# Kernel tuning notes

Hardware: AMD Instinct MI355X
Metric: run time of the kernel (lower is better)

Reference implementation:

```python
import jax, jax.numpy as jnp
import numpy as np


def _ortho_matrix(key, d, m):
    # block-orthogonal random matrix with chi-distributed row-norm rescaling
    n_blocks = m // d + (1 if m % d else 0)
    keys = jax.random.split(key, n_blocks + 1)
    blocks = []
    for i in range(m // d):
        q, _ = jnp.linalg.qr(jax.random.normal(keys[i], (d, d), dtype=jnp.float32))
        blocks.append(q)
    rem = m % d
    if rem > 0:
        q, _ = jnp.linalg.qr(jax.random.normal(keys[m // d], (d, d), dtype=jnp.float32))
        blocks.append(q[:, :rem])
    proj = jnp.concatenate(blocks, axis=1)  # [d, m]
    scales = jnp.linalg.norm(jax.random.normal(keys[-1], (m, d), dtype=jnp.float32), axis=1)
    return proj * scales[None, :]


def _feature_map(x, P, eps=1e-6):
    # FAVOR+ positive softmax feature map: [exp(xP - |x|^2/2), exp(-xP - |x|^2/2)]
    proj = x @ P  # [B,N,m]
    xn = 0.5 * jnp.sum(x * x, axis=-1, keepdims=True)
    pos = proj - xn
    neg = -proj - xn
    mx = jnp.maximum(jnp.max(pos, axis=-1, keepdims=True), jnp.max(neg, axis=-1, keepdims=True))
    feats = jnp.concatenate([jnp.exp(pos - mx), jnp.exp(neg - mx)], axis=-1)
    return feats * (2.0 * P.shape[1]) ** -0.5 + eps  # [B,N,2m]


def setup_inputs() -> dict:
    key = jax.random.key(0)
    ks = jax.random.split(key, 16)
    B, C, N = 4, 256, 8192
    da, nb = C // 4, 64
    d_geo, r_geo = 16, 16
    x = jax.random.normal(ks[0], (B, C, N), dtype=jnp.float32)
    pos = jax.random.uniform(ks[1], (B, N, 3), dtype=jnp.float32)
    Wq = jax.random.normal(ks[2], (da, C), dtype=jnp.float32) * (C ** -0.5)
    Wk = jax.random.normal(ks[3], (da, C), dtype=jnp.float32) * (C ** -0.5)
    Wv = jax.random.normal(ks[4], (C, C), dtype=jnp.float32) * (C ** -0.5)
    proj_sm = _ortho_matrix(ks[5], da, nb)  # [da, nb]
    Wg1 = jax.random.normal(ks[6], (d_geo, 3), dtype=jnp.float32) * (3 ** -0.5)
    bg1 = jnp.zeros((d_geo,), dtype=jnp.float32)
    Wg2 = jax.random.normal(ks[7], (d_geo, d_geo), dtype=jnp.float32) * (d_geo ** -0.5)
    bg2 = jnp.zeros((d_geo,), dtype=jnp.float32)
    log_tau = jnp.zeros((), dtype=jnp.float32)
    omega_geo = _ortho_matrix(ks[8], d_geo, r_geo)  # [d_geo, r_geo]
    Wp = jax.random.normal(ks[9], (C, C), dtype=jnp.float32) * (C ** -0.5)
    bn_gamma = jnp.ones((C,), dtype=jnp.float32)
    bn_beta = jnp.zeros((C,), dtype=jnp.float32)
    return {"x": x, "pos": pos, "Wq": Wq, "Wk": Wk, "Wv": Wv, "proj_sm": proj_sm,
            "Wg1": Wg1, "bg1": bg1, "Wg2": Wg2, "bg2": bg2, "log_tau": log_tau,
            "omega_geo": omega_geo, "Wp": Wp, "bn_gamma": bn_gamma, "bn_beta": bn_beta}


def reference(x, pos, Wq, Wk, Wv, proj_sm, Wg1, bg1, Wg2, bg2, log_tau, omega_geo, Wp, bn_gamma, bn_beta):
    eps = 1e-6
    da = Wq.shape[0]
    scale = da ** -0.25
    # 1x1 convs == channel matmuls; transpose to [B,N,*]
    q = jnp.einsum('bcn,oc->bno', x, Wq) * scale
    k = jnp.einsum('bcn,oc->bno', x, Wk) * scale
    v = jnp.einsum('bcn,oc->bno', x, Wv)
    q_p = _feature_map(q, proj_sm, eps)  # [B,N,r_sm]
    k_p = _feature_map(k, proj_sm, eps)
    # GeoRFF: learnable Gaussian RFF on MLP-transformed coordinates
    g = jax.nn.relu(pos @ Wg1.T + bg1) @ Wg2.T + bg2  # [B,N,d_geo]
    tau = jax.nn.softplus(log_tau) + 1e-6
    z = jnp.sqrt(2.0 * tau) * g
    z_proj = z @ omega_geo  # [B,N,r_geo]
    z_norm = 0.5 * jnp.sum(z * z, axis=-1, keepdims=True)
    phi = jnp.exp(z_proj - z_norm) * (omega_geo.shape[1] ** -0.5)  # [B,N,r_geo]
    # outer-product feature combination
    B, N, r_sm = q_p.shape
    r_geo = phi.shape[-1]
    Phi_q = (q_p[..., :, None] * phi[..., None, :]).reshape(B, N, r_sm * r_geo)
    Phi_k = (k_p[..., :, None] * phi[..., None, :]).reshape(B, N, r_sm * r_geo)
    # O(N) linear-attention chain
    kv = jnp.einsum('bnr,bnc->brc', Phi_k, v)         # [B,r,C]
    k_sum = jnp.sum(Phi_k, axis=1)                     # [B,r]
    denom = jnp.einsum('bnr,br->bn', Phi_q, k_sum)[..., None] + eps
    fsa = jnp.einsum('bnr,brc->bnc', Phi_q, kv) / denom  # [B,N,C]
    # offset attention: proj(x - fsa) + x, proj = Conv1x1 -> BN(train stats) -> ReLU
    y = x - jnp.transpose(fsa, (0, 2, 1))  # [B,C,N]
    h = jnp.einsum('bcn,oc->bon', y, Wp)
    mean = jnp.mean(h, axis=(0, 2), keepdims=True)
    var = jnp.var(h, axis=(0, 2), keepdims=True)
    hn = (h - mean) * jax.lax.rsqrt(var + 1e-5) * bn_gamma[None, :, None] + bn_beta[None, :, None]
    return jax.nn.relu(hn) + x
```

## Files before the change

### kernel.cpp

```cpp
#include <hip/hip_runtime.h>
#include <hip/hip_bf16.h>
#include <math.h>

#define BB 4
#define CC 256
#define NN 8192
#define RSM 128
#define RGEO 16

typedef __attribute__((ext_vector_type(8))) short short8v;
typedef __attribute__((ext_vector_type(4))) float f32x4;
typedef __attribute__((ext_vector_type(4))) unsigned int u32x4;

#define MFMA16 __builtin_amdgcn_mfma_f32_16x16x32_bf16

#define P_QP   0ull
#define P_KPT  8388608ull
#define P_PHIR 16777216ull
#define P_PHIT 17825792ull
#define P_XT   18874368ull
#define P_VT   35651584ull
#define P_YNT  35651584ull
#define P_KVT  56623104ull
#define P_DEN  61865984ull
#define P_WQK  61997056ull
#define P_WV   62062592ull
#define P_WP   62193664ull
#define P_PSMT 62324736ull
#define P_BN   62332928ull
#define P_KVF  62337024ull
#define P_H    0ull

__device__ __forceinline__ unsigned short f2bu(float f){
    __hip_bfloat16 h = __float2bfloat16(f);
    return __builtin_bit_cast(unsigned short, h);
}
__device__ __forceinline__ float bu2f(unsigned short u){
    return __builtin_bit_cast(float, ((unsigned int)u) << 16);
}
__device__ __forceinline__ unsigned int pack2(float a, float b){
    return (unsigned int)f2bu(a) | (((unsigned int)f2bu(b)) << 16);
}
__device__ __forceinline__ int swz128(int row, int cb){ return (row*128 + cb) ^ ((row & 7) << 4); }
__device__ __forceinline__ int swz256(int row, int cb){ return (row*256 + cb) ^ ((row & 7) << 4); }

__device__ __forceinline__ void stage64(const unsigned short* __restrict__ g, size_t stride,
                                        char* lds, int t){
    #pragma unroll
    for (int i = 0; i < 2; ++i){
        int id = t + 256*i; int row = id >> 3, q = id & 7;
        short8v v = *(const short8v*)(g + (size_t)row*stride + q*8);
        *(short8v*)(lds + swz128(row, q*16)) = v;
    }
}
__device__ __forceinline__ short8v fld(const char* lds, int row, int cb){
    return *(const short8v*)(lds + swz128(row, cb));
}
__device__ __forceinline__ void mfma8(const char* As, const char* Bs, f32x4 acc[2][2],
                                      int wm, int wn, int lr, int lq){
    #pragma unroll
    for (int kk = 0; kk < 2; ++kk){
        short8v a0 = fld(As, wm*32 + lr,      kk*64 + lq*16);
        short8v a1 = fld(As, wm*32 + 16 + lr, kk*64 + lq*16);
        short8v b0 = fld(Bs, wn*32 + lr,      kk*64 + lq*16);
        short8v b1 = fld(Bs, wn*32 + 16 + lr, kk*64 + lq*16);
        acc[0][0] = MFMA16(a0, b0, acc[0][0], 0, 0, 0);
        acc[0][1] = MFMA16(a0, b1, acc[0][1], 0, 0, 0);
        acc[1][0] = MFMA16(a1, b0, acc[1][0], 0, 0, 0);
        acc[1][1] = MFMA16(a1, b1, acc[1][1], 0, 0, 0);
    }
}

__global__ __launch_bounds__(256) void k_prep(const float* __restrict__ Wq, const float* __restrict__ Wk,
    const float* __restrict__ Wv, const float* __restrict__ Wp, const float* __restrict__ Psm,
    unsigned short* __restrict__ Wqk_bf, unsigned short* __restrict__ Wv_bf,
    unsigned short* __restrict__ Wp_bf, unsigned short* __restrict__ Psm_t,
    unsigned short* __restrict__ v_t)
{
    const int tid = blockIdx.x*256 + threadIdx.x;
    const int nth = 64*256;
    for (int i = tid; i < 32768; i += nth){
        int o = i >> 8, c = i & 255;
        Wqk_bf[i] = f2bu(o < 64 ? Wq[o*256 + c] : Wk[(o-64)*256 + c]);
    }
    for (int i = tid; i < 65536; i += nth) Wv_bf[i] = f2bu(Wv[i]);
    for (int i = tid; i < 65536; i += nth) Wp_bf[i] = f2bu(Wp[i]);
    for (int i = tid; i < 4096; i += nth){
        int m = i >> 6, o = i & 63;
        Psm_t[i] = f2bu(Psm[o*64 + m] * 0.35355339059327373f);
    }
    for (int i = tid; i < BB*64*NN; i += nth){
        int b = i >> 19, rem = i & 524287;
        int row = rem >> 13, n = rem & 8191;
        v_t[((size_t)(b*320 + 256 + row))*NN + n] = (row == 0) ? (unsigned short)0x3F80 : (unsigned short)0;
    }
}

__global__ __launch_bounds__(256) void k_xt(const float* __restrict__ x, unsigned short* __restrict__ xT)
{
    __shared__ float xs[64][65];
    const int t = threadIdx.x;
    const int b  = blockIdx.x >> 9;
    const int ct = (blockIdx.x >> 7) & 3;
    const int nt = blockIdx.x & 127;
    const int c0 = ct*64, n0 = nt*64;
    #pragma unroll
    for (int i = 0; i < 4; ++i){
        int id = t + 256*i; int row = id >> 4, fq = id & 15;
        f32x4 v = *(const f32x4*)(x + ((size_t)(b*CC + c0 + row))*NN + n0 + fq*4);
        xs[row][fq*4+0] = v[0]; xs[row][fq*4+1] = v[1];
        xs[row][fq*4+2] = v[2]; xs[row][fq*4+3] = v[3];
    }
    __syncthreads();
    #pragma unroll
    for (int i = 0; i < 2; ++i){
        int id = t + 256*i; int n = id >> 3, q = id & 7;
        u32x4 o;
        #pragma unroll
        for (int j2 = 0; j2 < 4; ++j2)
            o[j2] = pack2(xs[q*8 + j2*2][n], xs[q*8 + j2*2+1][n]);
        *(u32x4*)(void*)(xT + ((size_t)(b*NN + n0 + n))*CC + c0 + q*8) = o;
    }
}

__global__ __launch_bounds__(256) void k_wgemm(const unsigned short* __restrict__ A,
    const unsigned short* __restrict__ Bsrc, unsigned short* __restrict__ out, int orows)
{
    __shared__ __align__(16) char As[8192];
    __shared__ __align__(16) char Bs[8192];
    const int t = threadIdx.x;
    const int l = t & 63, w = t >> 6, wm = w >> 1, wn = w & 1, lr = l & 15, lq = l >> 4;
    const int b  = blockIdx.x >> 9;
    const int ct = (blockIdx.x >> 7) & 3;
    const int nt = blockIdx.x & 127;
    const int c0 = ct*64, n0 = nt*64;

    f32x4 acc[2][2] = {};
    for (int ks = 0; ks < 4; ++ks){
        stage64(A + (size_t)c0*256 + ks*64, 256, As, t);
        stage64(Bsrc + ((size_t)(b*NN + n0))*256 + ks*64, 256, Bs, t);
        __syncthreads();
        mfma8(As, Bs, acc, wm, wn, lr, lq);
        __syncthreads();
    }
    #pragma unroll
    for (int mi = 0; mi < 2; ++mi)
        #pragma unroll
        for (int ni = 0; ni < 2; ++ni)
            #pragma unroll
            for (int r = 0; r < 4; ++r){
                int c = c0 + wm*32 + mi*16 + lq*4 + r;
                int n = n0 + wn*32 + ni*16 + lr;
                out[((size_t)(b*orows + c))*NN + n] = f2bu(acc[mi][ni][r]);
            }
}

__global__ __launch_bounds__(256) void k_qk(const unsigned short* __restrict__ Wqk,
    const unsigned short* __restrict__ xT, const unsigned short* __restrict__ Psm_t,
    unsigned short* __restrict__ qp, unsigned short* __restrict__ kp_t)
{
    __shared__ __align__(16) char As[16384];
    __shared__ __align__(16) char Bs[8192];
    __shared__ __align__(16) char Ts[16384];
    __shared__ __align__(16) char Ps[8192];
    const int t = threadIdx.x;
    const int l = t & 63, w = t >> 6, wm = w >> 1, wn = w & 1, lr = l & 15, lq = l >> 4;
    const int b  = blockIdx.x >> 7;
    const int nt = blockIdx.x & 127;
    const int n0 = nt*64;

    stage64(Psm_t, 64, Ps, t);

    f32x4 acc[4][2] = {};
    for (int ks = 0; ks < 4; ++ks){
        #pragma unroll
        for (int i = 0; i < 4; ++i){
            int id = t + 256*i; int row = id >> 3, q = id & 7;
            short8v v = *(const short8v*)(Wqk + (size_t)row*256 + ks*64 + q*8);
            *(short8v*)(As + swz128(row, q*16)) = v;
        }
        stage64(xT + ((size_t)(b*NN + n0))*256 + ks*64, 256, Bs, t);
        __syncthreads();
        #pragma unroll
        for (int kk = 0; kk < 2; ++kk){
            short8v b0 = fld(Bs, wn*32 + lr,      kk*64 + lq*16);
            short8v b1 = fld(Bs, wn*32 + 16 + lr, kk*64 + lq*16);
            #pragma unroll
            for (int mi = 0; mi < 4; ++mi){
                short8v a = fld(As, wm*64 + mi*16 + lr, kk*64 + lq*16);
                acc[mi][0] = MFMA16(a, b0, acc[mi][0], 0, 0, 0);
                acc[mi][1] = MFMA16(a, b1, acc[mi][1], 0, 0, 0);
            }
        }
        __syncthreads();
    }
    #pragma unroll
    for (int mi = 0; mi < 4; ++mi)
        #pragma unroll
        for (int ni = 0; ni < 2; ++ni){
            int op = (wm*64 + mi*16 + lq*4)*2;
            int nrow = wn*32 + ni*16 + lr;
            *(unsigned int*)(Ts + swz256(nrow, op))     = pack2(acc[mi][ni][0], acc[mi][ni][1]);
            *(unsigned int*)(Ts + swz256(nrow, op + 4)) = pack2(acc[mi][ni][2], acc[mi][ni][3]);
        }
    __syncthreads();

    const float inv128 = 0.08838834764831845f;
    for (int p = 0; p < 2; ++p){
        f32x4 ac[4] = {};
        #pragma unroll
        for (int kk = 0; kk < 2; ++kk){
            short8v bf = *(const short8v*)(Ts + swz256(w*16 + lr, p*128 + kk*64 + lq*16));
            #pragma unroll
            for (int mi = 0; mi < 4; ++mi){
                short8v a = *(const short8v*)(Ps + swz128(mi*16 + lr, kk*64 + lq*16));
                ac[mi] = MFMA16(a, bf, ac[mi], 0, 0, 0);
            }
        }
        float mx = 0.f;
        #pragma unroll
        for (int mi = 0; mi < 4; ++mi)
            #pragma unroll
            for (int r = 0; r < 4; ++r) mx = fmaxf(mx, fabsf(ac[mi][r]));
        mx = fmaxf(mx, __shfl_xor(mx, 16));
        mx = fmaxf(mx, __shfl_xor(mx, 32));
        const int n = n0 + w*16 + lr;
        if (p == 0){
            unsigned short* qr = qp + ((size_t)(b*NN + n))*RSM;
            #pragma unroll
            for (int mi = 0; mi < 4; ++mi){
                float e0 = __expf( ac[mi][0]-mx)*inv128 + 1e-6f;
                float e1 = __expf( ac[mi][1]-mx)*inv128 + 1e-6f;
                float e2 = __expf( ac[mi][2]-mx)*inv128 + 1e-6f;
                float e3 = __expf( ac[mi][3]-mx)*inv128 + 1e-6f;
                float g0 = __expf(-ac[mi][0]-mx)*inv128 + 1e-6f;
                float g1 = __expf(-ac[mi][1]-mx)*inv128 + 1e-6f;
                float g2 = __expf(-ac[mi][2]-mx)*inv128 + 1e-6f;
                float g3 = __expf(-ac[mi][3]-mx)*inv128 + 1e-6f;
                int i0 = mi*16 + lq*4;
                uint2 pu; pu.x = pack2(e0, e1); pu.y = pack2(e2, e3);
                uint2 nu; nu.x = pack2(g0, g1); nu.y = pack2(g2, g3);
                *(uint2*)(void*)(qr + i0)      = pu;
                *(uint2*)(void*)(qr + 64 + i0) = nu;
            }
        } else {
            unsigned short* kb = kp_t + (size_t)(b*RSM)*NN + n;
            #pragma unroll
            for (int mi = 0; mi < 4; ++mi){
                int i0 = mi*16 + lq*4;
                #pragma unroll
                for (int r = 0; r < 4; ++r){
                    kb[(size_t)(i0 + r)*NN]      = f2bu(__expf( ac[mi][r]-mx)*inv128 + 1e-6f);
                    kb[(size_t)(i0 + r + 64)*NN] = f2bu(__expf(-ac[mi][r]-mx)*inv128 + 1e-6f);
                }
            }
        }
    }
}

__global__ __launch_bounds__(256) void k_phi(const float* __restrict__ pos,
    const float* __restrict__ Wg1, const float* __restrict__ bg1,
    const float* __restrict__ Wg2, const float* __restrict__ bg2,
    const float* __restrict__ log_tau, const float* __restrict__ omega,
    unsigned short* __restrict__ phi_row, unsigned short* __restrict__ phi_t)
{
    const int t = threadIdx.x;
    const int b = blockIdx.x >> 5;
    const int n = ((blockIdx.x & 31) << 8) + t;
    const float* pp = pos + ((size_t)(b*NN + n))*3;
    const float p0 = pp[0], p1 = pp[1], p2 = pp[2];
    float hb[16];
    #pragma unroll
    for (int i = 0; i < 16; ++i)
        hb[i] = fmaxf(0.f, fmaf(Wg1[i*3+0], p0, fmaf(Wg1[i*3+1], p1, fmaf(Wg1[i*3+2], p2, bg1[i]))));
    const float tau = log1pf(__expf(log_tau[0])) + 1e-6f;
    const float sc  = sqrtf(2.f*tau);
    float z[16]; float zn = 0.f;
    #pragma unroll
    for (int i = 0; i < 16; ++i){
        float g = bg2[i];
        #pragma unroll
        for (int j = 0; j < 16; ++j) g = fmaf(Wg2[i*16+j], hb[j], g);
        z[i] = sc*g; zn = fmaf(z[i], z[i], zn);
    }
    zn *= 0.5f;
    float val[16];
    #pragma unroll
    for (int m = 0; m < 16; ++m){
        float s = 0.f;
        #pragma unroll
        for (int i = 0; i < 16; ++i) s = fmaf(z[i], omega[i*16+m], s);
        val[m] = __expf(s - zn)*0.25f;
    }
    unsigned short* pr = phi_row + ((size_t)(b*NN + n))*16;
    u32x4 o0, o1;
    #pragma unroll
    for (int j2 = 0; j2 < 4; ++j2){
        o0[j2] = pack2(val[j2*2], val[j2*2+1]);
        o1[j2] = pack2(val[8+j2*2], val[8+j2*2+1]);
    }
    *(u32x4*)(void*)pr = o0;
    *(u32x4*)(void*)(pr + 8) = o1;
    #pragma unroll
    for (int m = 0; m < 16; ++m)
        phi_t[((size_t)(b*RGEO + m))*NN + n] = f2bu(val[m]);
}

__global__ __launch_bounds__(256) void k_kv(const unsigned short* __restrict__ kp_t,
    const unsigned short* __restrict__ phi_t, const unsigned short* __restrict__ v_t,
    float* __restrict__ kv_f32)
{
    __shared__ __align__(16) char As[8192];
    __shared__ __align__(16) char Bs[8192];
    const int t = threadIdx.x;
    const int l = t & 63, w = t >> 6, wm = w >> 1, wn = w & 1, lr = l & 15, lq = l >> 4;
    const int bid = blockIdx.x;
    const int b   = bid / 640;
    const int rem = bid % 640;
    const int ksl = rem / 160;
    const int rr  = rem % 160;
    const int ct = rr >> 5, rt = rr & 31;
    const int c0 = ct*64, r0 = rt*64;
    const int rl = t >> 2, u = t & 3;
    const int rg = r0 + rl;
    const unsigned short* kpr = kp_t + ((size_t)(b*RSM  + (rg >> 4)))*NN;
    const unsigned short* phr = phi_t + ((size_t)(b*RGEO + (rg & 15)))*NN;

    f32x4 acc[2][2] = {};
    for (int ks = ksl*32; ks < ksl*32 + 32; ++ks){
        const int nk = ks*64;
        stage64(v_t + ((size_t)(b*320 + c0))*NN + nk, NN, As, t);
        {
            const int nb = nk + u*16;
            short8v k0 = *(const short8v*)(kpr + nb);
            short8v k1 = *(const short8v*)(kpr + nb + 8);
            short8v q0 = *(const short8v*)(phr + nb);
            short8v q1 = *(const short8v*)(phr + nb + 8);
            u32x4 o0, o1;
            #pragma unroll
            for (int j2 = 0; j2 < 4; ++j2){
                o0[j2] = pack2(bu2f((unsigned short)k0[j2*2])  *bu2f((unsigned short)q0[j2*2]),
                               bu2f((unsigned short)k0[j2*2+1])*bu2f((unsigned short)q0[j2*2+1]));
                o1[j2] = pack2(bu2f((unsigned short)k1[j2*2])  *bu2f((unsigned short)q1[j2*2]),
                               bu2f((unsigned short)k1[j2*2+1])*bu2f((unsigned short)q1[j2*2+1]));
            }
            *(u32x4*)(Bs + swz128(rl, u*32))      = o0;
            *(u32x4*)(Bs + swz128(rl, u*32 + 16)) = o1;
        }
        __syncthreads();
        mfma8(As, Bs, acc, wm, wn, lr, lq);
        __syncthreads();
    }
    #pragma unroll
    for (int mi = 0; mi < 2; ++mi)
        #pragma unroll
        for (int ni = 0; ni < 2; ++ni)
            #pragma unroll
            for (int r = 0; r < 4; ++r){
                int c = c0 + wm*32 + mi*16 + lq*4 + r;
                int rg2 = r0 + wn*32 + ni*16 + lr;
                atomicAdd(&kv_f32[((size_t)(b*320 + c))*2048 + rg2], acc[mi][ni][r]);
            }
}

__global__ __launch_bounds__(256) void k_kvred(const float* __restrict__ kv_f32,
    unsigned short* __restrict__ kv_t)
{
    const size_t i = ((size_t)blockIdx.x*256 + threadIdx.x)*4;
    f32x4 v = *(const f32x4*)(kv_f32 + i);
    uint2 o; o.x = pack2(v[0], v[1]); o.y = pack2(v[2], v[3]);
    *(uint2*)(void*)(kv_t + i) = o;
}

__global__ __launch_bounds__(256) void k_denom(const unsigned short* __restrict__ qp,
    const unsigned short* __restrict__ phi_row, const unsigned short* __restrict__ kv_t,
    float* __restrict__ den)
{
    __shared__ float ks[2048];
    const int t = threadIdx.x;
    const int b = blockIdx.x >> 5;
    const int n = ((blockIdx.x & 31) << 8) + t;
    const unsigned short* ksrc = kv_t + ((size_t)(b*320 + 256))*2048;
    #pragma unroll
    for (int i = 0; i < 8; ++i){ int idx = t + 256*i; ks[idx] = bu2f(ksrc[idx]); }
    __syncthreads();
    float phf[16];
    {
        const unsigned short* pr = phi_row + ((size_t)(b*NN + n))*16;
        short8v a = *(const short8v*)pr;
        short8v c = *(const short8v*)(pr + 8);
        #pragma unroll
        for (int j = 0; j < 8; ++j){ phf[j] = bu2f((unsigned short)a[j]); phf[8+j] = bu2f((unsigned short)c[j]); }
    }
    const unsigned short* qr = qp + ((size_t)(b*NN + n))*RSM;
    float acc = 0.f;
    for (int i = 0; i < 128; i += 8){
        short8v qv = *(const short8v*)(qr + i);
        #pragma unroll
        for (int ii = 0; ii < 8; ++ii){
            const float* kk = &ks[(i + ii)*16];
            float s = 0.f;
            #pragma unroll
            for (int j = 0; j < 16; ++j) s = fmaf(phf[j], kk[j], s);
            acc = fmaf(bu2f((unsigned short)qv[ii]), s, acc);
        }
    }
    den[b*NN + n] = acc + 1e-6f;
}

__global__ __launch_bounds__(256) void k_fsa(const unsigned short* __restrict__ kv_t,
    const unsigned short* __restrict__ qp, const unsigned short* __restrict__ phi_row,
    const float* __restrict__ den, const unsigned short* __restrict__ xT,
    unsigned short* __restrict__ y_nt)
{
    __shared__ __align__(16) char As[8192];
    __shared__ __align__(16) char Bs[8192];
    __shared__ __align__(16) char Ys[8192];
    const int t = threadIdx.x;
    const int l = t & 63, w = t >> 6, wm = w >> 1, wn = w & 1, lr = l & 15, lq = l >> 4;
    const int b  = blockIdx.x >> 9;
    const int ct = (blockIdx.x >> 7) & 3;
    const int nt = blockIdx.x & 127;
    const int c0 = ct*64, n0 = nt*64;
    const int nl = t >> 2, u = t & 3;

    float phf[16];
    {
        const unsigned short* pr = phi_row + ((size_t)(b*NN + n0 + nl))*16;
        short8v a = *(const short8v*)pr;
        short8v c = *(const short8v*)(pr + 8);
        #pragma unroll
        for (int j = 0; j < 8; ++j){ phf[j] = bu2f((unsigned short)a[j]); phf[8+j] = bu2f((unsigned short)c[j]); }
    }
    const unsigned short* qprow = qp + ((size_t)(b*NN + n0 + nl))*RSM;

    f32x4 acc[2][2] = {};
    for (int ks = 0; ks < 32; ++ks){
        stage64(kv_t + ((size_t)(b*320 + c0))*2048 + ks*64, 2048, As, t);
        {
            float qv = bu2f(qprow[ks*4 + u]);
            u32x4 o0, o1;
            #pragma unroll
            for (int j2 = 0; j2 < 4; ++j2){
                o0[j2] = pack2(qv*phf[j2*2],     qv*phf[j2*2+1]);
                o1[j2] = pack2(qv*phf[8+j2*2],   qv*phf[8+j2*2+1]);
            }
            *(u32x4*)(Bs + swz128(nl, u*32))      = o0;
            *(u32x4*)(Bs + swz128(nl, u*32 + 16)) = o1;
        }
        __syncthreads();
        mfma8(As, Bs, acc, wm, wn, lr, lq);
        __syncthreads();
    }
    #pragma unroll
    for (int ni = 0; ni < 2; ++ni){
        float rd = 1.0f / den[(size_t)b*NN + n0 + wn*32 + ni*16 + lr];
        #pragma unroll
        for (int mi = 0; mi < 2; ++mi){
            int cb = (wm*32 + mi*16 + lq*4)*2;
            int nrow = wn*32 + ni*16 + lr;
            *(unsigned int*)(Ys + swz128(nrow, cb))     = pack2(acc[mi][ni][0]*rd, acc[mi][ni][1]*rd);
            *(unsigned int*)(Ys + swz128(nrow, cb + 4)) = pack2(acc[mi][ni][2]*rd, acc[mi][ni][3]*rd);
        }
    }
    __syncthreads();
    #pragma unroll
    for (int i = 0; i < 2; ++i){
        int q = u + i*4;
        short8v fs = *(const short8v*)(Ys + swz128(nl, q*16));
        short8v xv = *(const short8v*)(xT + ((size_t)(b*NN + n0 + nl))*CC + c0 + q*8);
        u32x4 o;
        #pragma unroll
        for (int j2 = 0; j2 < 4; ++j2){
            float y0 = bu2f((unsigned short)xv[j2*2])   - bu2f((unsigned short)fs[j2*2]);
            float y1 = bu2f((unsigned short)xv[j2*2+1]) - bu2f((unsigned short)fs[j2*2+1]);
            o[j2] = pack2(y0, y1);
        }
        *(u32x4*)(void*)(y_nt + ((size_t)(b*NN + n0 + nl))*CC + c0 + q*8) = o;
    }
}

__global__ __launch_bounds__(256) void k_bnstat(const unsigned short* __restrict__ h,
    const float* __restrict__ gamma, const float* __restrict__ beta, float* __restrict__ bn)
{
    __shared__ float s1[256], s2[256];
    const int t = threadIdx.x, c = blockIdx.x;
    float a1 = 0.f, a2 = 0.f;
    for (int b = 0; b < 4; ++b){
        const unsigned short* hr = h + ((size_t)(b*CC + c))*NN;
        #pragma unroll
        for (int i = 0; i < 4; ++i){
            short8v v = *(const short8v*)(hr + (t + i*256)*8);
            #pragma unroll
            for (int j = 0; j < 8; ++j){ float f = bu2f((unsigned short)v[j]); a1 += f; a2 = fmaf(f, f, a2); }
        }
    }
    s1[t] = a1; s2[t] = a2; __syncthreads();
    for (int st = 128; st > 0; st >>= 1){
        if (t < st){ s1[t] += s1[t + st]; s2[t] += s2[t + st]; }
        __syncthreads();
    }
    if (t == 0){
        float inv = 1.f/32768.f;
        float mean = s1[0]*inv, var = s2[0]*inv - mean*mean;
        float sc = gamma[c]*rsqrtf(var + 1e-5f);
        bn[512 + c] = sc; bn[768 + c] = fmaf(-mean, sc, beta[c]);
    }
}

__global__ __launch_bounds__(256) void k_apply(const unsigned short* __restrict__ h,
    const float* __restrict__ x, const float* __restrict__ bn, float* __restrict__ out)
{
    const size_t tot8 = (size_t)BB*CC*NN/8;
    for (size_t i = (size_t)blockIdx.x*256 + threadIdx.x; i < tot8; i += 2048*256){
        int c = (int)((i >> 10) & 255);
        float s = bn[512 + c], bb = bn[768 + c];
        short8v hv = *(const short8v*)(h + i*8);
        f32x4 x0 = *(const f32x4*)(x + i*8);
        f32x4 x1 = *(const f32x4*)(x + i*8 + 4);
        f32x4 o0, o1;
        #pragma unroll
        for (int j = 0; j < 4; ++j){
            o0[j] = fmaxf(fmaf(bu2f((unsigned short)hv[j]),     s, bb), 0.f) + x0[j];
            o1[j] = fmaxf(fmaf(bu2f((unsigned short)hv[4 + j]), s, bb), 0.f) + x1[j];
        }
        *(f32x4*)(out + i*8)     = o0;
        *(f32x4*)(out + i*8 + 4) = o1;
    }
}

extern "C" void kernel_launch(void* const* d_in, const int* in_sizes, int n_in,
                              void* d_out, int out_size, void* d_ws, size_t ws_size,
                              hipStream_t stream)
{
    (void)in_sizes; (void)n_in; (void)out_size; (void)ws_size;
    const float* x       = (const float*)d_in[0];
    const float* pos     = (const float*)d_in[1];
    const float* Wq      = (const float*)d_in[2];
    const float* Wk      = (const float*)d_in[3];
    const float* Wv      = (const float*)d_in[4];
    const float* Psm     = (const float*)d_in[5];
    const float* Wg1     = (const float*)d_in[6];
    const float* bg1     = (const float*)d_in[7];
    const float* Wg2     = (const float*)d_in[8];
    const float* bg2     = (const float*)d_in[9];
    const float* log_tau = (const float*)d_in[10];
    const float* omega   = (const float*)d_in[11];
    const float* Wp      = (const float*)d_in[12];
    const float* gamma   = (const float*)d_in[13];
    const float* beta    = (const float*)d_in[14];
    char* W = (char*)d_ws;
    float* out = (float*)d_out;

    unsigned short* qp    = (unsigned short*)(W + P_QP);
    unsigned short* kp_t  = (unsigned short*)(W + P_KPT);
    unsigned short* phir  = (unsigned short*)(W + P_PHIR);
    unsigned short* phit  = (unsigned short*)(W + P_PHIT);
    unsigned short* xT    = (unsigned short*)(W + P_XT);
    unsigned short* v_t   = (unsigned short*)(W + P_VT);
    unsigned short* y_nt  = (unsigned short*)(W + P_YNT);
    unsigned short* kv_t  = (unsigned short*)(W + P_KVT);
    float*          den   = (float*)(W + P_DEN);
    unsigned short* Wqk_b = (unsigned short*)(W + P_WQK);
    unsigned short* Wv_b  = (unsigned short*)(W + P_WV);
    unsigned short* Wp_b  = (unsigned short*)(W + P_WP);
    unsigned short* Psm_t = (unsigned short*)(W + P_PSMT);
    float*          bn    = (float*)(W + P_BN);
    float*          kvf   = (float*)(W + P_KVF);
    unsigned short* hbuf  = (unsigned short*)(W + P_H);

    hipMemsetAsync(W + P_KVF, 0, 10485760, stream);
    k_prep  <<<  64, 256, 0, stream>>>(Wq, Wk, Wv, Wp, Psm, Wqk_b, Wv_b, Wp_b, Psm_t, v_t);
    k_xt    <<<2048, 256, 0, stream>>>(x, xT);
    k_wgemm <<<2048, 256, 0, stream>>>(Wv_b, xT, v_t, 320);
    k_qk    <<< 512, 256, 0, stream>>>(Wqk_b, xT, Psm_t, qp, kp_t);
    k_phi   <<< 128, 256, 0, stream>>>(pos, Wg1, bg1, Wg2, bg2, log_tau, omega, phir, phit);
    k_kv    <<<2560, 256, 0, stream>>>(kp_t, phit, v_t, kvf);
    k_kvred <<<2560, 256, 0, stream>>>(kvf, kv_t);
    k_denom <<< 128, 256, 0, stream>>>(qp, phir, kv_t, den);
    k_fsa   <<<2048, 256, 0, stream>>>(kv_t, qp, phir, den, xT, y_nt);
    k_wgemm <<<2048, 256, 0, stream>>>(Wp_b, y_nt, hbuf, 256);
    k_bnstat<<< 256, 256, 0, stream>>>(hbuf, gamma, beta, bn);
    k_apply <<<2048, 256, 0, stream>>>(hbuf, x, bn, out);
}
```

Before: 353.7 us.

## Enlarge kv/fsa GEMM tiles to 128x128 and compute k_sum directly

The kv and fsa GEMM kernels move from 64x64 to 128x128 output tiles with a 4x4 MFMA fragment per wave, raising operand reuse and cutting the number of blocks and atomics. The appended ones-row trick that computed k_sum through the GEMM (320-row v_t) is replaced by a direct scalar reduction into a separate ksum buffer inside k_kv. This also removes the k_prep fill of the extra rows and shrinks the memset. In exchange, LDS use and register pressure per block rise, and fewer blocks may lower occupancy.

```diff
diff --git a/kernel.cpp b/kernel.cpp
--- a/kernel.cpp
+++ b/kernel.cpp
@@ -21,14 +21,15 @@
 #define P_XT   18874368ull
 #define P_VT   35651584ull
 #define P_YNT  35651584ull
-#define P_KVT  56623104ull
-#define P_DEN  61865984ull
-#define P_WQK  61997056ull
-#define P_WV   62062592ull
-#define P_WP   62193664ull
-#define P_PSMT 62324736ull
-#define P_BN   62332928ull
-#define P_KVF  62337024ull
+#define P_KVT  52428800ull
+#define P_KVF  56623104ull
+#define P_KSUM 65011712ull
+#define P_DEN  65044480ull
+#define P_WQK  65175552ull
+#define P_WV   65241088ull
+#define P_WP   65372160ull
+#define P_PSMT 65503232ull
+#define P_BN   65511424ull
 #define P_H    0ull
 
 __device__ __forceinline__ unsigned short f2bu(float f){
@@ -48,6 +49,15 @@
                                         char* lds, int t){
     #pragma unroll
     for (int i = 0; i < 2; ++i){
+        int id = t + 256*i; int row = id >> 3, q = id & 7;
+        short8v v = *(const short8v*)(g + (size_t)row*stride + q*8);
+        *(short8v*)(lds + swz128(row, q*16)) = v;
+    }
+}
+__device__ __forceinline__ void stage128(const unsigned short* __restrict__ g, size_t stride,
+                                         char* lds, int t){
+    #pragma unroll
+    for (int i = 0; i < 4; ++i){
         int id = t + 256*i; int row = id >> 3, q = id & 7;
         short8v v = *(const short8v*)(g + (size_t)row*stride + q*8);
         *(short8v*)(lds + swz128(row, q*16)) = v;
@@ -70,12 +80,27 @@
         acc[1][1] = MFMA16(a1, b1, acc[1][1], 0, 0, 0);
     }
 }
+__device__ __forceinline__ void mfma16s(const char* As, const char* Bs, f32x4 acc[4][4],
+                                        int wm, int wn, int lr, int lq){
+    #pragma unroll
+    for (int kk = 0; kk < 2; ++kk){
+        short8v af[4], bf[4];
+        #pragma unroll
+        for (int f = 0; f < 4; ++f) af[f] = fld(As, wm*64 + f*16 + lr, kk*64 + lq*16);
+        #pragma unroll
+        for (int f = 0; f < 4; ++f) bf[f] = fld(Bs, wn*64 + f*16 + lr, kk*64 + lq*16);
+        #pragma unroll
+        for (int fa = 0; fa < 4; ++fa)
+            #pragma unroll
+            for (int fb = 0; fb < 4; ++fb)
+                acc[fa][fb] = MFMA16(af[fa], bf[fb], acc[fa][fb], 0, 0, 0);
+    }
+}
 
 __global__ __launch_bounds__(256) void k_prep(const float* __restrict__ Wq, const float* __restrict__ Wk,
     const float* __restrict__ Wv, const float* __restrict__ Wp, const float* __restrict__ Psm,
     unsigned short* __restrict__ Wqk_bf, unsigned short* __restrict__ Wv_bf,
-    unsigned short* __restrict__ Wp_bf, unsigned short* __restrict__ Psm_t,
-    unsigned short* __restrict__ v_t)
+    unsigned short* __restrict__ Wp_bf, unsigned short* __restrict__ Psm_t)
 {
     const int tid = blockIdx.x*256 + threadIdx.x;
     const int nth = 64*256;
@@ -88,11 +113,6 @@
     for (int i = tid; i < 4096; i += nth){
         int m = i >> 6, o = i & 63;
         Psm_t[i] = f2bu(Psm[o*64 + m] * 0.35355339059327373f);
-    }
-    for (int i = tid; i < BB*64*NN; i += nth){
-        int b = i >> 19, rem = i & 524287;
-        int row = rem >> 13, n = rem & 8191;
-        v_t[((size_t)(b*320 + 256 + row))*NN + n] = (row == 0) ? (unsigned short)0x3F80 : (unsigned short)0;
     }
 }
 
@@ -308,59 +328,75 @@
 
 __global__ __launch_bounds__(256) void k_kv(const unsigned short* __restrict__ kp_t,
     const unsigned short* __restrict__ phi_t, const unsigned short* __restrict__ v_t,
-    float* __restrict__ kv_f32)
-{
-    __shared__ __align__(16) char As[8192];
-    __shared__ __align__(16) char Bs[8192];
+    float* __restrict__ kv_f32, float* __restrict__ ksum)
+{
+    __shared__ __align__(16) char As[16384];
+    __shared__ __align__(16) char Bs[16384];
     const int t = threadIdx.x;
     const int l = t & 63, w = t >> 6, wm = w >> 1, wn = w & 1, lr = l & 15, lq = l >> 4;
     const int bid = blockIdx.x;
-    const int b   = bid / 640;
-    const int rem = bid % 640;
-    const int ksl = rem / 160;
-    const int rr  = rem % 160;
-    const int ct = rr >> 5, rt = rr & 31;
-    const int c0 = ct*64, r0 = rt*64;
-    const int rl = t >> 2, u = t & 3;
-    const int rg = r0 + rl;
+    const int rt  = bid & 15;
+    const int ct  = (bid >> 4) & 1;
+    const int ksl = (bid >> 5) & 7;
+    const int b   = bid >> 8;
+    const int c0 = ct*128, r0 = rt*128;
+
+    const int brow = t >> 1, half = t & 1;
+    const int rg = r0 + brow;
     const unsigned short* kpr = kp_t + ((size_t)(b*RSM  + (rg >> 4)))*NN;
     const unsigned short* phr = phi_t + ((size_t)(b*RGEO + (rg & 15)))*NN;
-
-    f32x4 acc[2][2] = {};
-    for (int ks = ksl*32; ks < ksl*32 + 32; ++ks){
-        const int nk = ks*64;
-        stage64(v_t + ((size_t)(b*320 + c0))*NN + nk, NN, As, t);
+    float ksacc = 0.f;
+
+    f32x4 acc[4][4] = {};
+    for (int ks = 0; ks < 16; ++ks){
+        const int nk = ksl*1024 + ks*64;
+        stage128(v_t + ((size_t)(b*CC + c0))*NN + nk, NN, As, t);
         {
-            const int nb = nk + u*16;
-            short8v k0 = *(const short8v*)(kpr + nb);
-            short8v k1 = *(const short8v*)(kpr + nb + 8);
-            short8v q0 = *(const short8v*)(phr + nb);
-            short8v q1 = *(const short8v*)(phr + nb + 8);
-            u32x4 o0, o1;
-            #pragma unroll
-            for (int j2 = 0; j2 < 4; ++j2){
-                o0[j2] = pack2(bu2f((unsigned short)k0[j2*2])  *bu2f((unsigned short)q0[j2*2]),
-                               bu2f((unsigned short)k0[j2*2+1])*bu2f((unsigned short)q0[j2*2+1]));
-                o1[j2] = pack2(bu2f((unsigned short)k1[j2*2])  *bu2f((unsigned short)q1[j2*2]),
-                               bu2f((unsigned short)k1[j2*2+1])*bu2f((unsigned short)q1[j2*2+1]));
-            }
-            *(u32x4*)(Bs + swz128(rl, u*32))      = o0;
-            *(u32x4*)(Bs + swz128(rl, u*32 + 16)) = o1;
-        }
-        __syncthreads();
-        mfma8(As, Bs, acc, wm, wn, lr, lq);
-        __syncthreads();
-    }
-    #pragma unroll
-    for (int mi = 0; mi < 2; ++mi)
-        #pragma unroll
-        for (int ni = 0; ni < 2; ++ni)
-            #pragma unroll
-            for (int r = 0; r < 4; ++r){
-                int c = c0 + wm*32 + mi*16 + lq*4 + r;
-                int rg2 = r0 + wn*32 + ni*16 + lr;
-                atomicAdd(&kv_f32[((size_t)(b*320 + c))*2048 + rg2], acc[mi][ni][r]);
-            }
+            const int nb = nk + half*32;
+            #pragma unroll
+            for (int c4 = 0; c4 < 2; ++c4){
+                short8v k0 = *(const short8v*)(kpr + nb + c4*16);
+                short8v k1 = *(const short8v*)(kpr + nb + c4*16 + 8);
+                short8v p0 = *(const short8v*)(phr + nb + c4*16);
+                short8v p1 = *(const short8v*)(phr + nb + c4*16 + 8);
+                float pr0[8], pr1[8];
+                #pragma unroll
+                for (int e = 0; e < 8; ++e){
+                    pr0[e] = bu2f((unsigned short)k0[e])*bu2f((unsigned short)p0[e]);
+                    pr1[e] = bu2f((unsigned short)k1[e])*bu2f((unsigned short)p1[e]);
+                }
+                if (ct == 0){
+                    #pragma unroll
+                    for (int e = 0; e < 8; ++e) ksacc += pr0[e] + pr1[e];
+                }
+                u32x4 o0, o1;
+                #pragma unroll
+                for (int j2 = 0; j2 < 4; ++j2){
+                    o0[j2] = pack2(pr0[j2*2], pr0[j2*2+1]);
+                    o1[j2] = pack2(pr1[j2*2], pr1[j2*2+1]);
+                }
+                *(u32x4*)(Bs + swz128(brow, half*64 + c4*32))      = o0;
+                *(u32x4*)(Bs + swz128(brow, half*64 + c4*32 + 16)) = o1;
+            }
+        }
+        __syncthreads();
+        mfma16s(As, Bs, acc, wm, wn, lr, lq);
+        __syncthreads();
+    }
+    #pragma unroll
+    for (int fa = 0; fa < 4; ++fa)
+        #pragma unroll
+        for (int fb = 0; fb < 4; ++fb)
+            #pragma unroll
+            for (int e = 0; e < 4; ++e){
+                int c = c0 + wm*64 + fa*16 + lq*4 + e;
+                int r = r0 + wn*64 + fb*16 + lr;
+                atomicAdd(&kv_f32[((size_t)(b*CC + c))*2048 + r], acc[fa][fb][e]);
+            }
+    if (ct == 0){
+        float o = __shfl_xor(ksacc, 1);
+        if (half == 0) atomicAdd(&ksum[b*2048 + rg], ksacc + o);
+    }
 }
 
 __global__ __launch_bounds__(256) void k_kvred(const float* __restrict__ kv_f32,
@@ -373,16 +409,16 @@
 }
 
 __global__ __launch_bounds__(256) void k_denom(const unsigned short* __restrict__ qp,
-    const unsigned short* __restrict__ phi_row, const unsigned short* __restrict__ kv_t,
+    const unsigned short* __restrict__ phi_row, const float* __restrict__ ksum,
     float* __restrict__ den)
 {
     __shared__ float ks[2048];
     const int t = threadIdx.x;
     const int b = blockIdx.x >> 5;
     const int n = ((blockIdx.x & 31) << 8) + t;
-    const unsigned short* ksrc = kv_t + ((size_t)(b*320 + 256))*2048;
-    #pragma unroll
-    for (int i = 0; i < 8; ++i){ int idx = t + 256*i; ks[idx] = bu2f(ksrc[idx]); }
+    const float* ksrc = ksum + b*2048;
+    #pragma unroll
+    for (int i = 0; i < 8; ++i){ int idx = t + 256*i; ks[idx] = ksrc[idx]; }
     __syncthreads();
     float phf[16];
     {
@@ -413,62 +449,74 @@
     const float* __restrict__ den, const unsigned short* __restrict__ xT,
     unsigned short* __restrict__ y_nt)
 {
-    __shared__ __align__(16) char As[8192];
-    __shared__ __align__(16) char Bs[8192];
-    __shared__ __align__(16) char Ys[8192];
+    __shared__ __align__(16) char Sm[32768];
+    char* As = Sm;
+    char* Bs = Sm + 16384;
     const int t = threadIdx.x;
     const int l = t & 63, w = t >> 6, wm = w >> 1, wn = w & 1, lr = l & 15, lq = l >> 4;
-    const int b  = blockIdx.x >> 9;
-    const int ct = (blockIdx.x >> 7) & 3;
-    const int nt = blockIdx.x & 127;
-    const int c0 = ct*64, n0 = nt*64;
-    const int nl = t >> 2, u = t & 3;
-
+    const int nt = blockIdx.x & 63;
+    const int ct = (blockIdx.x >> 6) & 1;
+    const int b  = blockIdx.x >> 7;
+    const int c0 = ct*128, n0 = nt*128;
+
+    const int brow = t >> 1, half = t & 1;
     float phf[16];
     {
-        const unsigned short* pr = phi_row + ((size_t)(b*NN + n0 + nl))*16;
+        const unsigned short* pr = phi_row + ((size_t)(b*NN + n0 + brow))*16;
         short8v a = *(const short8v*)pr;
         short8v c = *(const short8v*)(pr + 8);
         #pragma unroll
         for (int j = 0; j < 8; ++j){ phf[j] = bu2f((unsigned short)a[j]); phf[8+j] = bu2f((unsigned short)c[j]); }
     }
-    const unsigned short* qprow = qp + ((size_t)(b*NN + n0 + nl))*RSM;
-
-    f32x4 acc[2][2] = {};
+    const unsigned short* qrow = qp + ((size_t)(b*NN + n0 + brow))*RSM;
+
+    f32x4 acc[4][4] = {};
     for (int ks = 0; ks < 32; ++ks){
-        stage64(kv_t + ((size_t)(b*320 + c0))*2048 + ks*64, 2048, As, t);
+        const int rk = ks*64;
+        stage128(kv_t + ((size_t)(b*CC + c0))*2048 + rk, 2048, As, t);
         {
-            float qv = bu2f(qprow[ks*4 + u]);
-            u32x4 o0, o1;
+            const int ib = (rk >> 4) + half*2;
+            const float q0 = bu2f(qrow[ib]);
+            const float q1 = bu2f(qrow[ib + 1]);
+            u32x4 oa, ob;
             #pragma unroll
             for (int j2 = 0; j2 < 4; ++j2){
-                o0[j2] = pack2(qv*phf[j2*2],     qv*phf[j2*2+1]);
-                o1[j2] = pack2(qv*phf[8+j2*2],   qv*phf[8+j2*2+1]);
-            }
-            *(u32x4*)(Bs + swz128(nl, u*32))      = o0;
-            *(u32x4*)(Bs + swz128(nl, u*32 + 16)) = o1;
-        }
-        __syncthreads();
-        mfma8(As, Bs, acc, wm, wn, lr, lq);
-        __syncthreads();
-    }
-    #pragma unroll
-    for (int ni = 0; ni < 2; ++ni){
-        float rd = 1.0f / den[(size_t)b*NN + n0 + wn*32 + ni*16 + lr];
-        #pragma unroll
-        for (int mi = 0; mi < 2; ++mi){
-            int cb = (wm*32 + mi*16 + lq*4)*2;
-            int nrow = wn*32 + ni*16 + lr;
-            *(unsigned int*)(Ys + swz128(nrow, cb))     = pack2(acc[mi][ni][0]*rd, acc[mi][ni][1]*rd);
-            *(unsigned int*)(Ys + swz128(nrow, cb + 4)) = pack2(acc[mi][ni][2]*rd, acc[mi][ni][3]*rd);
-        }
-    }
+                oa[j2] = pack2(q0*phf[j2*2],     q0*phf[j2*2+1]);
+                ob[j2] = pack2(q0*phf[8+j2*2],   q0*phf[8+j2*2+1]);
+            }
+            *(u32x4*)(Bs + swz128(brow, half*64))      = oa;
+            *(u32x4*)(Bs + swz128(brow, half*64 + 16)) = ob;
+            #pragma unroll
+            for (int j2 = 0; j2 < 4; ++j2){
+                oa[j2] = pack2(q1*phf[j2*2],     q1*phf[j2*2+1]);
+                ob[j2] = pack2(q1*phf[8+j2*2],   q1*phf[8+j2*2+1]);
+            }
+            *(u32x4*)(Bs + swz128(brow, half*64 + 32)) = oa;
+            *(u32x4*)(Bs + swz128(brow, half*64 + 48)) = ob;
+        }
+        __syncthreads();
+        mfma16s(As, Bs, acc, wm, wn, lr, lq);
+        __syncthreads();
+    }
+    float rd[4];
+    #pragma unroll
+    for (int fb = 0; fb < 4; ++fb)
+        rd[fb] = 1.0f / den[(size_t)b*NN + n0 + wn*64 + fb*16 + lr];
+    #pragma unroll
+    for (int fa = 0; fa < 4; ++fa)
+        #pragma unroll
+        for (int fb = 0; fb < 4; ++fb){
+            int nrow = wn*64 + fb*16 + lr;
+            int cb   = (wm*64 + fa*16 + lq*4)*2;
+            *(unsigned int*)(Sm + swz256(nrow, cb))     = pack2(acc[fa][fb][0]*rd[fb], acc[fa][fb][1]*rd[fb]);
+            *(unsigned int*)(Sm + swz256(nrow, cb + 4)) = pack2(acc[fa][fb][2]*rd[fb], acc[fa][fb][3]*rd[fb]);
+        }
     __syncthreads();
     #pragma unroll
-    for (int i = 0; i < 2; ++i){
-        int q = u + i*4;
-        short8v fs = *(const short8v*)(Ys + swz128(nl, q*16));
-        short8v xv = *(const short8v*)(xT + ((size_t)(b*NN + n0 + nl))*CC + c0 + q*8);
+    for (int i = 0; i < 8; ++i){
+        int id = t + 256*i; int row = id >> 4, q = id & 15;
+        short8v fs = *(const short8v*)(Sm + swz256(row, q*16));
+        short8v xv = *(const short8v*)(xT + ((size_t)(b*NN + n0 + row))*CC + c0 + q*8);
         u32x4 o;
         #pragma unroll
         for (int j2 = 0; j2 < 4; ++j2){
@@ -476,7 +524,7 @@
             float y1 = bu2f((unsigned short)xv[j2*2+1]) - bu2f((unsigned short)fs[j2*2+1]);
             o[j2] = pack2(y0, y1);
         }
-        *(u32x4*)(void*)(y_nt + ((size_t)(b*NN + n0 + nl))*CC + c0 + q*8) = o;
+        *(u32x4*)(void*)(y_nt + ((size_t)(b*NN + n0 + row))*CC + c0 + q*8) = o;
     }
 }
 
@@ -560,25 +608,26 @@
     unsigned short* v_t   = (unsigned short*)(W + P_VT);
     unsigned short* y_nt  = (unsigned short*)(W + P_YNT);
     unsigned short* kv_t  = (unsigned short*)(W + P_KVT);
+    float*          kvf   = (float*)(W + P_KVF);
+    float*          ksum  = (float*)(W + P_KSUM);
     float*          den   = (float*)(W + P_DEN);
     unsigned short* Wqk_b = (unsigned short*)(W + P_WQK);
     unsigned short* Wv_b  = (unsigned short*)(W + P_WV);
     unsigned short* Wp_b  = (unsigned short*)(W + P_WP);
     unsigned short* Psm_t = (unsigned short*)(W + P_PSMT);
     float*          bn    = (float*)(W + P_BN);
-    float*          kvf   = (float*)(W + P_KVF);
     unsigned short* hbuf  = (unsigned short*)(W + P_H);
 
-    hipMemsetAsync(W + P_KVF, 0, 10485760, stream);
-    k_prep  <<<  64, 256, 0, stream>>>(Wq, Wk, Wv, Wp, Psm, Wqk_b, Wv_b, Wp_b, Psm_t, v_t);
+    hipMemsetAsync(W + P_KVF, 0, 8421376, stream);
+    k_prep  <<<  64, 256, 0, stream>>>(Wq, Wk, Wv, Wp, Psm, Wqk_b, Wv_b, Wp_b, Psm_t);
     k_xt    <<<2048, 256, 0, stream>>>(x, xT);
-    k_wgemm <<<2048, 256, 0, stream>>>(Wv_b, xT, v_t, 320);
+    k_wgemm <<<2048, 256, 0, stream>>>(Wv_b, xT, v_t, 256);
     k_qk    <<< 512, 256, 0, stream>>>(Wqk_b, xT, Psm_t, qp, kp_t);
     k_phi   <<< 128, 256, 0, stream>>>(pos, Wg1, bg1, Wg2, bg2, log_tau, omega, phir, phit);
-    k_kv    <<<2560, 256, 0, stream>>>(kp_t, phit, v_t, kvf);
-    k_kvred <<<2560, 256, 0, stream>>>(kvf, kv_t);
-    k_denom <<< 128, 256, 0, stream>>>(qp, phir, kv_t, den);
-    k_fsa   <<<2048, 256, 0, stream>>>(kv_t, qp, phir, den, xT, y_nt);
+    k_kv    <<<1024, 256, 0, stream>>>(kp_t, phit, v_t, kvf, ksum);
+    k_kvred <<<2048, 256, 0, stream>>>(kvf, kv_t);
+    k_denom <<< 128, 256, 0, stream>>>(qp, phir, ksum, den);
+    k_fsa   <<< 512, 256, 0, stream>>>(kv_t, qp, phir, den, xT, y_nt);
     k_wgemm <<<2048, 256, 0, stream>>>(Wp_b, y_nt, hbuf, 256);
     k_bnstat<<< 256, 256, 0, stream>>>(hbuf, gamma, beta, bn);
     k_apply <<<2048, 256, 0, stream>>>(hbuf, x, bn, out);
```

New measurement: 330.0 us. 1.07x faster.
